# Kernel tuning notes

Measured on AMD Instinct MI355X. Metric: run time of the kernel, lower is better.

The kernel has to match this reference:

```python
import jax, jax.numpy as jnp
import numpy as np

SCALE, K, PATCH, STRIDE = 2, 5, 3, 1
EPS = 1e-5


def im2patch(x, p, s):
    # x: (b,c,H,W) -> (b,c,p,p,m1,m2), 'VALID' patches (padding is 0 for our sizes)
    b, c, H, W = x.shape
    m1 = (H - p) // s + 1
    m2 = (W - p) // s + 1
    ii = (jnp.arange(m1) * s)[:, None] + jnp.arange(p)[None, :]   # (m1,p)
    jj = (jnp.arange(m2) * s)[:, None] + jnp.arange(p)[None, :]   # (m2,p)
    pt = x[:, :, ii[:, :, None, None], jj[None, None, :, :]]      # (b,c,m1,p,m2,p)
    return pt.transpose(0, 1, 3, 5, 2, 4)                         # (b,c,p,p,m1,m2)


def patch2im(patches, p, s):
    # overlap-add fold, averaged by per-pixel patch counts (torch F.fold / ones-fold divisor)
    b, c, _, _, m1, m2 = patches.shape
    Hp = (m1 - 1) * s + p
    Wp = (m2 - 1) * s + p
    out = jnp.zeros((b, c, Hp, Wp), patches.dtype)
    cnt = jnp.zeros((Hp, Wp), patches.dtype)
    for i in range(p):          # fixed small loop over patch offsets (p*p = 36)
        for j in range(p):
            out = out.at[:, :, i:i + s * m1:s, j:j + s * m2:s].add(patches[:, :, i, j])
            cnt = cnt.at[i:i + s * m1:s, j:j + s * m2:s].add(1.0)
    return out / cnt


def setup_inputs():
    key = jax.random.key(0)
    k1, k2, k3 = jax.random.split(key, 3)
    b, cy, H, W = 1, 64, 80, 80
    y = jax.random.normal(k1, (b, cy, H, W), jnp.float32)
    yd = jax.random.normal(k2, (b, cy * SCALE ** 2, H // SCALE, W // SCALE), jnp.float32)
    m = ((H - PATCH) // STRIDE + 1) ** 2
    n = ((H // SCALE - PATCH) // STRIDE + 1) ** 2
    idx_k = jax.random.randint(k3, (b, m, K), 0, n, jnp.int32)
    return {"y": y, "yd": yd, "idx_k": idx_k}


def reference(y, yd, idx_k):
    b, cy, H, W = y.shape
    c = yd.shape[1]           # = cy * scale^2
    rs = SCALE ** 2
    y_p = im2patch(y, PATCH, STRIDE)      # (b,cy,p,p,m1,m2)
    yd_p = im2patch(yd, PATCH, STRIDE)    # (b,c,p,p,n1,n2)
    m1, m2 = y_p.shape[-2:]
    n1, n2 = yd_p.shape[-2:]
    m, n = m1 * m2, n1 * n2
    f = c * PATCH * PATCH
    y_flat = y_p.transpose(0, 4, 5, 1, 2, 3).reshape(b, m, f // rs)
    yd_flat = yd_p.transpose(0, 4, 5, 1, 2, 3).reshape(b, n, f)
    # top-k neighbor gather: (b,n,f)[idx (b,m,k)] -> (b,m,k,f) -> (b,m,f,k)
    z = jax.vmap(lambda t, i: t[i])(yd_flat, idx_k)
    z = z.transpose(0, 1, 3, 2)
    # AdaIN: normalize gathered HR patches, apply LR query patch stats (unbiased var, torch default)
    y_n = y_flat.reshape(b, m, c // rs, PATCH * PATCH)
    z_n = z.reshape(b, m, c // rs, rs * PATCH * PATCH, K)
    z_mu = z_n.mean(axis=3, keepdims=True)
    z_sd = jnp.sqrt(z_n.var(axis=3, ddof=1, keepdims=True) + EPS)
    y_mu = y_n.mean(axis=3, keepdims=True)[..., None]        # (b,m,c',1,1)
    y_sd = jnp.sqrt(y_n.var(axis=3, ddof=1, keepdims=True) + EPS)[..., None]
    z = ((z_n - z_mu) / z_sd * y_sd + y_mu).reshape(b, m, f, K)
    # rearrange f = (cy, scale, scale, p1, p2) into SR patches (b, k*cy, p*scale, p*scale, m1, m2)
    z = z.transpose(0, 3, 2, 1)                                   # (b,k,f,m)
    z = z.reshape(b, K, cy, SCALE, SCALE, PATCH, PATCH, m1, m2)
    z = z.transpose(0, 1, 2, 5, 3, 6, 4, 7, 8)                    # (b,k,cy,p1,s,p2,s,m1,m2)
    z = z.reshape(b, K * cy, PATCH * SCALE, PATCH * SCALE, m1, m2)
    z_sr = patch2im(z, PATCH * SCALE, STRIDE * SCALE)             # (b,k*cy,H*scale,W*scale)
    return z_sr.reshape(b, K * cy, H * SCALE, W * SCALE)
```

## Files before the change

kernel.cpp:

```cpp
#include <hip/hip_runtime.h>
#include <hip/hip_fp16.h>
#include <string.h>

#define CY     64
#define HY     80
#define HD     40
#define SPD    (HD*HD)
#define M1     78
#define N1     38
#define M_TOT  (M1*M1)
#define N_TOT  (N1*N1)
#define KK     5
#define HS     160
#define EPSF   1e-5f
#define LP     17

typedef float f32x2 __attribute__((ext_vector_type(2)));

__device__ __forceinline__ unsigned pkf16(float a, float b) {
    __half2 h = __floats2half2_rn(a, b);
    unsigned u; memcpy(&u, &h, 4); return u;
}
__device__ __forceinline__ f32x2 upk2(unsigned u) {
    __half2 h; memcpy(&h, &u, 4);
    float2 f = __half22float2(h);
    f32x2 r; r.x = f.x; r.y = f.y; return r;
}

__global__ __launch_bounds__(256) void pre_kernel(const float* __restrict__ y,
                                                  const float* __restrict__ yd,
                                                  uint4* __restrict__ ydW,
                                                  unsigned* __restrict__ zstP,
                                                  unsigned* __restrict__ ystP) {
    int id = blockIdx.x * 256 + threadIdx.x;
    if (id < SPD * 64) {
        int cc = id & 63, sp = id >> 6;
        const float* b0 = yd + (cc * 4) * SPD + sp;
        int d = (sp < SPD - 1) ? 1 : 0;
        ydW[sp * 64 + cc] = make_uint4(pkf16(b0[0], b0[SPD]),
                                       pkf16(b0[2*SPD], b0[3*SPD]),
                                       pkf16(b0[d], b0[SPD+d]),
                                       pkf16(b0[2*SPD+d], b0[3*SPD+d]));
        return;
    }
    id -= SPD * 64;
    if (id < N_TOT * 64) {
        int n  = id % N_TOT;
        int cc = id / N_TOT;
        int ni = n / N1, nj = n - ni * N1;
        const float* base = yd + (cc * 4) * SPD + ni * HD + nj;
        float s = 0.f, sq = 0.f;
#pragma unroll
        for (int r = 0; r < 4; ++r)
#pragma unroll
            for (int i = 0; i < 3; ++i)
#pragma unroll
                for (int j = 0; j < 3; ++j) {
                    float v = base[r * SPD + i * HD + j];
                    s += v; sq += v * v;
                }
        float mu  = s * (1.f / 36.f);
        float var = (sq - 36.f * mu * mu) * (1.f / 35.f);
        zstP[n * 64 + cc] = pkf16(mu, rsqrtf(var + EPSF));
        return;
    }
    id -= N_TOT * 64;
    if (id >= CY * M_TOT) return;
    int m  = id % M_TOT;
    int cc = id / M_TOT;
    int mi = m / M1, mj = m - mi * M1;
    const float* base = y + cc * (HY * HY) + mi * HY + mj;
    float s = 0.f, sq = 0.f;
#pragma unroll
    for (int i = 0; i < 3; ++i)
#pragma unroll
        for (int j = 0; j < 3; ++j) {
            float v = base[i * HY + j];
            s += v; sq += v * v;
        }
    float mu  = s * (1.f / 9.f);
    float var = (sq - 9.f * mu * mu) * (1.f / 8.f);
    ystP[m * 64 + cc] = pkf16(mu, sqrtf(var + EPSF));
}

__global__ __launch_bounds__(256) void agg_kernel(
    const uint4* __restrict__ ydW, const unsigned* __restrict__ zstP,
    const unsigned* __restrict__ ystP, const int* __restrict__ idx,
    float* __restrict__ out)
{
    __shared__ float lds[128 * LP];

    int lane = threadIdx.x & 63;
    int w    = __builtin_amdgcn_readfirstlane(threadIdx.x >> 6);
    int bid  = blockIdx.x;
    int wg   = (bid & 7) * 500 + (bid >> 3);
    int k    = wg / 800;
    int rem  = wg - k * 800;
    int y    = rem / 10;
    int xb   = rem - y * 10;
    int x0   = xb * 8 + w * 2;

    f32x2 acc01[2] = {{0.f,0.f},{0.f,0.f}};
    f32x2 acc23[2] = {{0.f,0.f},{0.f,0.f}};
    float bs[2] = {0.f, 0.f};
    float inv0, inv1;

    auto serve = [&](f32x2& a01, f32x2& a23, float& bsum,
                     unsigned lo, unsigned hi, float a, float b) {
        f32x2 am; am.x = a; am.y = a;
        a01 = __builtin_elementwise_fma(am, upk2(lo), a01);
        a23 = __builtin_elementwise_fma(am, upk2(hi), a23);
        bsum += b;
    };

    if (y >= 2 && y <= M1 - 1 && x0 >= 2 && x0 <= M1 - 2) {
        inv0 = inv1 = 1.f / 9.f;
        unsigned ysu[12], zsu[12];
        int nn[12];
#pragma unroll
        for (int p = 0; p < 12; ++p) {
            int m = (y - 2 + (p >> 2)) * M1 + (x0 - 2 + (p & 3));
            nn[p]  = idx[m * KK + k];
            ysu[p] = ystP[m * 64 + lane];
        }
#pragma unroll
        for (int p = 0; p < 12; ++p)
            zsu[p] = zstP[nn[p] * 64 + lane];
        float aa[12], bb[12];
        int spb[12];
#pragma unroll
        for (int p = 0; p < 12; ++p) {
            f32x2 ys = upk2(ysu[p]), zs = upk2(zsu[p]);
            aa[p] = ys.y * zs.y;
            bb[p] = fmaf(-zs.x, aa[p], ys.x);
            int n = nn[p], ni = n / N1;
            spb[p] = ni * HD + (n - ni * N1);
        }
#pragma unroll
        for (int r = 0; r < 3; ++r) {
            int roff = (2 - r) * HD;
            int s0 = spb[r*4+0] + roff, s1 = spb[r*4+1] + roff;
            int s2 = spb[r*4+2] + roff, s3 = spb[r*4+3] + roff;
            uint2 v0 = *(const uint2*)(ydW + (s0 + 2) * 64 + lane);
            uint4 v1 = ydW[(s1 + 1) * 64 + lane];
            uint4 v2 = ydW[(s2 + 0) * 64 + lane];
            uint2 v3 = *(const uint2*)(ydW + (s3 + 0) * 64 + lane);
            serve(acc01[0], acc23[0], bs[0], v0.x, v0.y, aa[r*4+0], bb[r*4+0]);
            serve(acc01[0], acc23[0], bs[0], v1.x, v1.y, aa[r*4+1], bb[r*4+1]);
            serve(acc01[1], acc23[1], bs[1], v1.z, v1.w, aa[r*4+1], bb[r*4+1]);
            serve(acc01[0], acc23[0], bs[0], v2.x, v2.y, aa[r*4+2], bb[r*4+2]);
            serve(acc01[1], acc23[1], bs[1], v2.z, v2.w, aa[r*4+2], bb[r*4+2]);
            serve(acc01[1], acc23[1], bs[1], v3.x, v3.y, aa[r*4+3], bb[r*4+3]);
        }
    } else {
#pragma unroll
        for (int q = 0; q < 2; ++q) {
            int x = x0 + q;
            int milo = max(0, y - 2), mihi = min(M1 - 1, y);
            int mjlo = max(0, x - 2), mjhi = min(M1 - 1, x);
            float iv = 1.f / (float)((mihi - milo + 1) * (mjhi - mjlo + 1));
            if (q == 0) inv0 = iv; else inv1 = iv;
            for (int mi = milo; mi <= mihi; ++mi)
                for (int mj = mjlo; mj <= mjhi; ++mj) {
                    int m = mi * M1 + mj;
                    int n = idx[m * KK + k];
                    f32x2 ys = upk2(ystP[m * 64 + lane]);
                    f32x2 zs = upk2(zstP[n * 64 + lane]);
                    float a = ys.y * zs.y;
                    float b = fmaf(-zs.x, a, ys.x);
                    int ni = n / N1;
                    int sp = ni * HD + (n - ni * N1) + (y - mi) * HD + (x - mj);
                    uint2 v = *(const uint2*)(ydW + sp * 64 + lane);
                    if (q == 0) serve(acc01[0], acc23[0], bs[0], v.x, v.y, a, b);
                    else        serve(acc01[1], acc23[1], bs[1], v.x, v.y, a, b);
                }
        }
    }

#pragma unroll
    for (int q = 0; q < 2; ++q) {
        float iv = q ? inv1 : inv0;
        float bq = bs[q];
        int col = (w * 2 + q) * 2;
        lds[(0 * CY + lane) * LP + col]     = (acc01[q].x + bq) * iv;
        lds[(0 * CY + lane) * LP + col + 1] = (acc01[q].y + bq) * iv;
        lds[(1 * CY + lane) * LP + col]     = (acc23[q].x + bq) * iv;
        lds[(1 * CY + lane) * LP + col + 1] = (acc23[q].y + bq) * iv;
    }

    __syncthreads();

    int q  = lane >> 4;
    int xi = lane & 15;
    int X0 = xb * 16, Y0 = 2 * y;
#pragma unroll
    for (int t = 0; t < 8; ++t) {
        int row = t * 16 + w * 4 + q;
        float v = lds[row * LP + xi];
        int dy = row >> 6, cc = row & 63;
        __builtin_nontemporal_store(v,
            out + (((size_t)(k * CY + cc) * HS + (Y0 + dy)) * HS + X0 + xi));
    }
}

extern "C" void kernel_launch(void* const* d_in, const int* in_sizes, int n_in,
                              void* d_out, int out_size, void* d_ws, size_t ws_size,
                              hipStream_t stream) {
    const float* y   = (const float*)d_in[0];
    const float* yd  = (const float*)d_in[1];
    const int*   idx = (const int*)d_in[2];
    float* out = (float*)d_out;

    char* ws = (char*)d_ws;
    uint4*    ydW  = (uint4*)ws;
    unsigned* zstP = (unsigned*)(ws + 1638400);
    unsigned* ystP = (unsigned*)(ws + 2008064);

    int pre_total = SPD * 64 + N_TOT * 64 + CY * M_TOT;
    pre_kernel<<<(pre_total + 255) / 256, 256, 0, stream>>>(y, yd, ydW, zstP, ystP);
    agg_kernel<<<KK * 800, 256, 0, stream>>>(ydW, zstP, ystP, idx, out);
}
```

Before: 32.40 us.

## Process two row tiles per block with early-issued gathers for the second tile

Each block of the aggregation kernel now handles two output rows (y0 and y0+40), which halves the grid. The index, statistics and feature loads for the second tile are issued before the first tile's compute and store phase, so their latency overlaps with that work. This is meant to hide gather latency and spread block launch overhead over more work. In exchange it raises register pressure, which may lower occupancy, and it adds an extra LDS barrier between the two store phases.

```diff
diff --git a/kernel.cpp b/kernel.cpp
--- a/kernel.cpp
+++ b/kernel.cpp
@@ -93,17 +93,40 @@
     int lane = threadIdx.x & 63;
     int w    = __builtin_amdgcn_readfirstlane(threadIdx.x >> 6);
     int bid  = blockIdx.x;
-    int wg   = (bid & 7) * 500 + (bid >> 3);
-    int k    = wg / 800;
-    int rem  = wg - k * 800;
-    int y    = rem / 10;
-    int xb   = rem - y * 10;
+    int wg   = (bid & 7) * 250 + (bid >> 3);
+    int k    = wg / 400;
+    int rem  = wg - k * 400;
+    int y0   = rem / 10;
+    int xb   = rem - y0 * 10;
     int x0   = xb * 8 + w * 2;
-
-    f32x2 acc01[2] = {{0.f,0.f},{0.f,0.f}};
-    f32x2 acc23[2] = {{0.f,0.f},{0.f,0.f}};
-    float bs[2] = {0.f, 0.f};
-    float inv0, inv1;
+    int yA   = y0, yB = y0 + 40;
+
+    bool fx    = (x0 >= 2 && x0 <= M1 - 2);
+    bool fastA = fx && (yA >= 2) && (yA <= M1 - 1);
+    bool fastB = fx && (yB >= 2) && (yB <= M1 - 1);
+
+    int nnA[12], nnB[12];
+    unsigned ysuA[12], ysuB[12], zsuA[12], zsuB[12];
+    if (fastA) {
+#pragma unroll
+        for (int p = 0; p < 12; ++p) {
+            int m = (yA - 2 + (p >> 2)) * M1 + (x0 - 2 + (p & 3));
+            nnA[p]  = idx[m * KK + k];
+            ysuA[p] = ystP[m * 64 + lane];
+        }
+#pragma unroll
+        for (int p = 0; p < 12; ++p) zsuA[p] = zstP[nnA[p] * 64 + lane];
+    }
+    if (fastB) {
+#pragma unroll
+        for (int p = 0; p < 12; ++p) {
+            int m = (yB - 2 + (p >> 2)) * M1 + (x0 - 2 + (p & 3));
+            nnB[p]  = idx[m * KK + k];
+            ysuB[p] = ystP[m * 64 + lane];
+        }
+#pragma unroll
+        for (int p = 0; p < 12; ++p) zsuB[p] = zstP[nnB[p] * 64 + lane];
+    }
 
     auto serve = [&](f32x2& a01, f32x2& a23, float& bsum,
                      unsigned lo, unsigned hi, float a, float b) {
@@ -113,53 +136,15 @@
         bsum += b;
     };
 
-    if (y >= 2 && y <= M1 - 1 && x0 >= 2 && x0 <= M1 - 2) {
-        inv0 = inv1 = 1.f / 9.f;
-        unsigned ysu[12], zsu[12];
-        int nn[12];
-#pragma unroll
-        for (int p = 0; p < 12; ++p) {
-            int m = (y - 2 + (p >> 2)) * M1 + (x0 - 2 + (p & 3));
-            nn[p]  = idx[m * KK + k];
-            ysu[p] = ystP[m * 64 + lane];
-        }
-#pragma unroll
-        for (int p = 0; p < 12; ++p)
-            zsu[p] = zstP[nn[p] * 64 + lane];
-        float aa[12], bb[12];
-        int spb[12];
-#pragma unroll
-        for (int p = 0; p < 12; ++p) {
-            f32x2 ys = upk2(ysu[p]), zs = upk2(zsu[p]);
-            aa[p] = ys.y * zs.y;
-            bb[p] = fmaf(-zs.x, aa[p], ys.x);
-            int n = nn[p], ni = n / N1;
-            spb[p] = ni * HD + (n - ni * N1);
-        }
-#pragma unroll
-        for (int r = 0; r < 3; ++r) {
-            int roff = (2 - r) * HD;
-            int s0 = spb[r*4+0] + roff, s1 = spb[r*4+1] + roff;
-            int s2 = spb[r*4+2] + roff, s3 = spb[r*4+3] + roff;
-            uint2 v0 = *(const uint2*)(ydW + (s0 + 2) * 64 + lane);
-            uint4 v1 = ydW[(s1 + 1) * 64 + lane];
-            uint4 v2 = ydW[(s2 + 0) * 64 + lane];
-            uint2 v3 = *(const uint2*)(ydW + (s3 + 0) * 64 + lane);
-            serve(acc01[0], acc23[0], bs[0], v0.x, v0.y, aa[r*4+0], bb[r*4+0]);
-            serve(acc01[0], acc23[0], bs[0], v1.x, v1.y, aa[r*4+1], bb[r*4+1]);
-            serve(acc01[1], acc23[1], bs[1], v1.z, v1.w, aa[r*4+1], bb[r*4+1]);
-            serve(acc01[0], acc23[0], bs[0], v2.x, v2.y, aa[r*4+2], bb[r*4+2]);
-            serve(acc01[1], acc23[1], bs[1], v2.z, v2.w, aa[r*4+2], bb[r*4+2]);
-            serve(acc01[1], acc23[1], bs[1], v3.x, v3.y, aa[r*4+3], bb[r*4+3]);
-        }
-    } else {
+    auto slow_tile = [&](int yt, f32x2 a01[2], f32x2 a23[2], float bs[2],
+                         float& i0, float& i1) {
 #pragma unroll
         for (int q = 0; q < 2; ++q) {
             int x = x0 + q;
-            int milo = max(0, y - 2), mihi = min(M1 - 1, y);
+            int milo = max(0, yt - 2), mihi = min(M1 - 1, yt);
             int mjlo = max(0, x - 2), mjhi = min(M1 - 1, x);
             float iv = 1.f / (float)((mihi - milo + 1) * (mjhi - mjlo + 1));
-            if (q == 0) inv0 = iv; else inv1 = iv;
+            if (q == 0) i0 = iv; else i1 = iv;
             for (int mi = milo; mi <= mihi; ++mi)
                 for (int mj = mjlo; mj <= mjhi; ++mj) {
                     int m = mi * M1 + mj;
@@ -169,37 +154,148 @@
                     float a = ys.y * zs.y;
                     float b = fmaf(-zs.x, a, ys.x);
                     int ni = n / N1;
-                    int sp = ni * HD + (n - ni * N1) + (y - mi) * HD + (x - mj);
+                    int sp = ni * HD + (n - ni * N1) + (yt - mi) * HD + (x - mj);
                     uint2 v = *(const uint2*)(ydW + sp * 64 + lane);
-                    if (q == 0) serve(acc01[0], acc23[0], bs[0], v.x, v.y, a, b);
-                    else        serve(acc01[1], acc23[1], bs[1], v.x, v.y, a, b);
+                    if (q == 0) serve(a01[0], a23[0], bs[0], v.x, v.y, a, b);
+                    else        serve(a01[1], a23[1], bs[1], v.x, v.y, a, b);
                 }
         }
-    }
-
-#pragma unroll
-    for (int q = 0; q < 2; ++q) {
-        float iv = q ? inv1 : inv0;
-        float bq = bs[q];
-        int col = (w * 2 + q) * 2;
-        lds[(0 * CY + lane) * LP + col]     = (acc01[q].x + bq) * iv;
-        lds[(0 * CY + lane) * LP + col + 1] = (acc01[q].y + bq) * iv;
-        lds[(1 * CY + lane) * LP + col]     = (acc23[q].x + bq) * iv;
-        lds[(1 * CY + lane) * LP + col + 1] = (acc23[q].y + bq) * iv;
-    }
-
-    __syncthreads();
-
-    int q  = lane >> 4;
-    int xi = lane & 15;
-    int X0 = xb * 16, Y0 = 2 * y;
-#pragma unroll
-    for (int t = 0; t < 8; ++t) {
-        int row = t * 16 + w * 4 + q;
-        float v = lds[row * LP + xi];
-        int dy = row >> 6, cc = row & 63;
-        __builtin_nontemporal_store(v,
-            out + (((size_t)(k * CY + cc) * HS + (Y0 + dy)) * HS + X0 + xi));
+    };
+
+    f32x2 accA01[2] = {{0.f,0.f},{0.f,0.f}};
+    f32x2 accA23[2] = {{0.f,0.f},{0.f,0.f}};
+    float bsA[2] = {0.f, 0.f};
+    float invA0 = 1.f / 9.f, invA1 = 1.f / 9.f;
+    if (fastA) {
+        int spbA[12];
+#pragma unroll
+        for (int p = 0; p < 12; ++p) {
+            int n = nnA[p], ni = n / N1;
+            spbA[p] = ni * HD + (n - ni * N1);
+        }
+        uint2 Aw0[3], Aw3[3]; uint4 Au1[3], Au2[3];
+#pragma unroll
+        for (int r = 0; r < 3; ++r) {
+            int roff = (2 - r) * HD;
+            Aw0[r] = *(const uint2*)(ydW + (spbA[r*4+0] + roff + 2) * 64 + lane);
+            Au1[r] = ydW[(spbA[r*4+1] + roff + 1) * 64 + lane];
+            Au2[r] = ydW[(spbA[r*4+2] + roff + 0) * 64 + lane];
+            Aw3[r] = *(const uint2*)(ydW + (spbA[r*4+3] + roff + 0) * 64 + lane);
+        }
+#pragma unroll
+        for (int r = 0; r < 3; ++r) {
+            float aa0, bb0, aa1, bb1, aa2, bb2, aa3, bb3;
+            { f32x2 ys = upk2(ysuA[r*4+0]), zs = upk2(zsuA[r*4+0]);
+              aa0 = ys.y * zs.y; bb0 = fmaf(-zs.x, aa0, ys.x); }
+            { f32x2 ys = upk2(ysuA[r*4+1]), zs = upk2(zsuA[r*4+1]);
+              aa1 = ys.y * zs.y; bb1 = fmaf(-zs.x, aa1, ys.x); }
+            { f32x2 ys = upk2(ysuA[r*4+2]), zs = upk2(zsuA[r*4+2]);
+              aa2 = ys.y * zs.y; bb2 = fmaf(-zs.x, aa2, ys.x); }
+            { f32x2 ys = upk2(ysuA[r*4+3]), zs = upk2(zsuA[r*4+3]);
+              aa3 = ys.y * zs.y; bb3 = fmaf(-zs.x, aa3, ys.x); }
+            serve(accA01[0], accA23[0], bsA[0], Aw0[r].x, Aw0[r].y, aa0, bb0);
+            serve(accA01[0], accA23[0], bsA[0], Au1[r].x, Au1[r].y, aa1, bb1);
+            serve(accA01[1], accA23[1], bsA[1], Au1[r].z, Au1[r].w, aa1, bb1);
+            serve(accA01[0], accA23[0], bsA[0], Au2[r].x, Au2[r].y, aa2, bb2);
+            serve(accA01[1], accA23[1], bsA[1], Au2[r].z, Au2[r].w, aa2, bb2);
+            serve(accA01[1], accA23[1], bsA[1], Aw3[r].x, Aw3[r].y, aa3, bb3);
+        }
+    } else {
+        slow_tile(yA, accA01, accA23, bsA, invA0, invA1);
+    }
+
+    uint2 Bw0[3], Bw3[3]; uint4 Bu1[3], Bu2[3];
+    if (fastB) {
+        int spbB[12];
+#pragma unroll
+        for (int p = 0; p < 12; ++p) {
+            int n = nnB[p], ni = n / N1;
+            spbB[p] = ni * HD + (n - ni * N1);
+        }
+#pragma unroll
+        for (int r = 0; r < 3; ++r) {
+            int roff = (2 - r) * HD;
+            Bw0[r] = *(const uint2*)(ydW + (spbB[r*4+0] + roff + 2) * 64 + lane);
+            Bu1[r] = ydW[(spbB[r*4+1] + roff + 1) * 64 + lane];
+            Bu2[r] = ydW[(spbB[r*4+2] + roff + 0) * 64 + lane];
+            Bw3[r] = *(const uint2*)(ydW + (spbB[r*4+3] + roff + 0) * 64 + lane);
+        }
+    }
+
+    {
+#pragma unroll
+        for (int q = 0; q < 2; ++q) {
+            float iv = q ? invA1 : invA0;
+            float bq = bsA[q];
+            int col = (w * 2 + q) * 2;
+            lds[(0 * CY + lane) * LP + col]     = (accA01[q].x + bq) * iv;
+            lds[(0 * CY + lane) * LP + col + 1] = (accA01[q].y + bq) * iv;
+            lds[(1 * CY + lane) * LP + col]     = (accA23[q].x + bq) * iv;
+            lds[(1 * CY + lane) * LP + col + 1] = (accA23[q].y + bq) * iv;
+        }
+        __syncthreads();
+        int q = lane >> 4, xi = lane & 15;
+        int X0 = xb * 16, Y0 = 2 * yA;
+#pragma unroll
+        for (int t = 0; t < 8; ++t) {
+            int row = t * 16 + w * 4 + q;
+            float v = lds[row * LP + xi];
+            int dy = row >> 6, cc = row & 63;
+            __builtin_nontemporal_store(v,
+                out + (((size_t)(k * CY + cc) * HS + (Y0 + dy)) * HS + X0 + xi));
+        }
+        __syncthreads();
+    }
+
+    f32x2 accB01[2] = {{0.f,0.f},{0.f,0.f}};
+    f32x2 accB23[2] = {{0.f,0.f},{0.f,0.f}};
+    float bsB[2] = {0.f, 0.f};
+    float invB0 = 1.f / 9.f, invB1 = 1.f / 9.f;
+    if (fastB) {
+#pragma unroll
+        for (int r = 0; r < 3; ++r) {
+            float aa0, bb0, aa1, bb1, aa2, bb2, aa3, bb3;
+            { f32x2 ys = upk2(ysuB[r*4+0]), zs = upk2(zsuB[r*4+0]);
+              aa0 = ys.y * zs.y; bb0 = fmaf(-zs.x, aa0, ys.x); }
+            { f32x2 ys = upk2(ysuB[r*4+1]), zs = upk2(zsuB[r*4+1]);
+              aa1 = ys.y * zs.y; bb1 = fmaf(-zs.x, aa1, ys.x); }
+            { f32x2 ys = upk2(ysuB[r*4+2]), zs = upk2(zsuB[r*4+2]);
+              aa2 = ys.y * zs.y; bb2 = fmaf(-zs.x, aa2, ys.x); }
+            { f32x2 ys = upk2(ysuB[r*4+3]), zs = upk2(zsuB[r*4+3]);
+              aa3 = ys.y * zs.y; bb3 = fmaf(-zs.x, aa3, ys.x); }
+            serve(accB01[0], accB23[0], bsB[0], Bw0[r].x, Bw0[r].y, aa0, bb0);
+            serve(accB01[0], accB23[0], bsB[0], Bu1[r].x, Bu1[r].y, aa1, bb1);
+            serve(accB01[1], accB23[1], bsB[1], Bu1[r].z, Bu1[r].w, aa1, bb1);
+            serve(accB01[0], accB23[0], bsB[0], Bu2[r].x, Bu2[r].y, aa2, bb2);
+            serve(accB01[1], accB23[1], bsB[1], Bu2[r].z, Bu2[r].w, aa2, bb2);
+            serve(accB01[1], accB23[1], bsB[1], Bw3[r].x, Bw3[r].y, aa3, bb3);
+        }
+    } else {
+        slow_tile(yB, accB01, accB23, bsB, invB0, invB1);
+    }
+
+    {
+#pragma unroll
+        for (int q = 0; q < 2; ++q) {
+            float iv = q ? invB1 : invB0;
+            float bq = bsB[q];
+            int col = (w * 2 + q) * 2;
+            lds[(0 * CY + lane) * LP + col]     = (accB01[q].x + bq) * iv;
+            lds[(0 * CY + lane) * LP + col + 1] = (accB01[q].y + bq) * iv;
+            lds[(1 * CY + lane) * LP + col]     = (accB23[q].x + bq) * iv;
+            lds[(1 * CY + lane) * LP + col + 1] = (accB23[q].y + bq) * iv;
+        }
+        __syncthreads();
+        int q = lane >> 4, xi = lane & 15;
+        int X0 = xb * 16, Y0 = 2 * yB;
+#pragma unroll
+        for (int t = 0; t < 8; ++t) {
+            int row = t * 16 + w * 4 + q;
+            float v = lds[row * LP + xi];
+            int dy = row >> 6, cc = row & 63;
+            __builtin_nontemporal_store(v,
+                out + (((size_t)(k * CY + cc) * HS + (Y0 + dy)) * HS + X0 + xi));
+        }
     }
 }
 
@@ -218,5 +314,5 @@
 
     int pre_total = SPD * 64 + N_TOT * 64 + CY * M_TOT;
     pre_kernel<<<(pre_total + 255) / 256, 256, 0, stream>>>(y, yd, ydW, zstP, ystP);
-    agg_kernel<<<KK * 800, 256, 0, stream>>>(ydW, zstP, ystP, idx, out);
-}
+    agg_kernel<<<KK * 400, 256, 0, stream>>>(ydW, zstP, ystP, idx, out);
+}
```

New measurement: 35.64 us. 1.1x slower.

## Process two neighbor ranks per workgroup to share query stats and reduce blocks

Applied to the files above, without the earlier changes.

Each workgroup of the aggregation kernel now handles two of the K neighbor indices (the last group handles one), so the ystP query-statistics loads and the index arithmetic are shared across both. The grid shrinks from 4000 to 2400 blocks and the LDS tile doubles to hold both outputs. The cost is higher register pressure from doubled accumulators and in-flight gathers, which may lower occupancy, and an uneven load between the two-rank and one-rank blocks.

```diff
diff --git a/kernel.cpp b/kernel.cpp
--- a/kernel.cpp
+++ b/kernel.cpp
@@ -83,123 +83,161 @@
     ystP[m * 64 + cc] = pkf16(mu, sqrtf(var + EPSF));
 }
 
+template<int NK>
+__device__ __forceinline__ void tile_run(
+    int lane, int w, int k0, int y, int x0,
+    const uint4* __restrict__ ydW, const unsigned* __restrict__ zstP,
+    const unsigned* __restrict__ ystP, const int* __restrict__ idx,
+    float* lds, float inv[2])
+{
+    f32x2 acc01[NK][2], acc23[NK][2];
+    float bs[NK][2];
+#pragma unroll
+    for (int kk = 0; kk < NK; ++kk)
+#pragma unroll
+        for (int q = 0; q < 2; ++q) {
+            acc01[kk][q].x = 0.f; acc01[kk][q].y = 0.f;
+            acc23[kk][q].x = 0.f; acc23[kk][q].y = 0.f;
+            bs[kk][q] = 0.f;
+        }
+
+    auto serve = [&](int kk, int q, unsigned lo, unsigned hi, float a, float b) {
+        f32x2 am; am.x = a; am.y = a;
+        acc01[kk][q] = __builtin_elementwise_fma(am, upk2(lo), acc01[kk][q]);
+        acc23[kk][q] = __builtin_elementwise_fma(am, upk2(hi), acc23[kk][q]);
+        bs[kk][q] += b;
+    };
+
+    if (y >= 2 && y <= M1 - 1 && x0 >= 2 && x0 <= M1 - 2) {
+        inv[0] = inv[1] = 1.f / 9.f;
+        int nn[NK][12];
+        unsigned ysu[12];
+#pragma unroll
+        for (int p = 0; p < 12; ++p) {
+            int m = (y - 2 + (p >> 2)) * M1 + (x0 - 2 + (p & 3));
+#pragma unroll
+            for (int kk = 0; kk < NK; ++kk) nn[kk][p] = idx[m * KK + k0 + kk];
+            ysu[p] = ystP[m * 64 + lane];
+        }
+#pragma unroll
+        for (int r = 0; r < 3; ++r) {
+            int roff = (2 - r) * HD;
+            unsigned zsu[NK][4];
+            uint2 v0[NK], v3[NK]; uint4 u1[NK], u2[NK];
+#pragma unroll
+            for (int kk = 0; kk < NK; ++kk) {
+                int n0 = nn[kk][r*4+0], n1 = nn[kk][r*4+1];
+                int n2 = nn[kk][r*4+2], n3 = nn[kk][r*4+3];
+                int s0 = (n0 / N1) * HD + (n0 - (n0 / N1) * N1) + roff;
+                int s1 = (n1 / N1) * HD + (n1 - (n1 / N1) * N1) + roff;
+                int s2 = (n2 / N1) * HD + (n2 - (n2 / N1) * N1) + roff;
+                int s3 = (n3 / N1) * HD + (n3 - (n3 / N1) * N1) + roff;
+                v0[kk] = *(const uint2*)(ydW + (s0 + 2) * 64 + lane);
+                u1[kk] = ydW[(s1 + 1) * 64 + lane];
+                u2[kk] = ydW[(s2 + 0) * 64 + lane];
+                v3[kk] = *(const uint2*)(ydW + (s3 + 0) * 64 + lane);
+                zsu[kk][0] = zstP[n0 * 64 + lane];
+                zsu[kk][1] = zstP[n1 * 64 + lane];
+                zsu[kk][2] = zstP[n2 * 64 + lane];
+                zsu[kk][3] = zstP[n3 * 64 + lane];
+            }
+#pragma unroll
+            for (int kk = 0; kk < NK; ++kk) {
+                float aa[4], bb[4];
+#pragma unroll
+                for (int c = 0; c < 4; ++c) {
+                    f32x2 ys = upk2(ysu[r*4+c]), zs = upk2(zsu[kk][c]);
+                    aa[c] = ys.y * zs.y;
+                    bb[c] = fmaf(-zs.x, aa[c], ys.x);
+                }
+                serve(kk, 0, v0[kk].x, v0[kk].y, aa[0], bb[0]);
+                serve(kk, 0, u1[kk].x, u1[kk].y, aa[1], bb[1]);
+                serve(kk, 1, u1[kk].z, u1[kk].w, aa[1], bb[1]);
+                serve(kk, 0, u2[kk].x, u2[kk].y, aa[2], bb[2]);
+                serve(kk, 1, u2[kk].z, u2[kk].w, aa[2], bb[2]);
+                serve(kk, 1, v3[kk].x, v3[kk].y, aa[3], bb[3]);
+            }
+        }
+    } else {
+#pragma unroll
+        for (int q = 0; q < 2; ++q) {
+            int x = x0 + q;
+            int milo = max(0, y - 2), mihi = min(M1 - 1, y);
+            int mjlo = max(0, x - 2), mjhi = min(M1 - 1, x);
+            inv[q] = 1.f / (float)((mihi - milo + 1) * (mjhi - mjlo + 1));
+            for (int mi = milo; mi <= mihi; ++mi)
+                for (int mj = mjlo; mj <= mjhi; ++mj) {
+                    int m = mi * M1 + mj;
+                    unsigned ysuv = ystP[m * 64 + lane];
+#pragma unroll
+                    for (int kk = 0; kk < NK; ++kk) {
+                        int n = idx[m * KK + k0 + kk];
+                        f32x2 ys = upk2(ysuv);
+                        f32x2 zs = upk2(zstP[n * 64 + lane]);
+                        float a = ys.y * zs.y;
+                        float b = fmaf(-zs.x, a, ys.x);
+                        int ni = n / N1;
+                        int sp = ni * HD + (n - ni * N1) + (y - mi) * HD + (x - mj);
+                        uint2 v = *(const uint2*)(ydW + sp * 64 + lane);
+                        serve(kk, q, v.x, v.y, a, b);
+                    }
+                }
+        }
+    }
+
+#pragma unroll
+    for (int kk = 0; kk < NK; ++kk)
+#pragma unroll
+        for (int q = 0; q < 2; ++q) {
+            float iv = inv[q];
+            float bq = bs[kk][q];
+            int col = (w * 2 + q) * 2;
+            lds[((kk * 2 + 0) * CY + lane) * LP + col]     = (acc01[kk][q].x + bq) * iv;
+            lds[((kk * 2 + 0) * CY + lane) * LP + col + 1] = (acc01[kk][q].y + bq) * iv;
+            lds[((kk * 2 + 1) * CY + lane) * LP + col]     = (acc23[kk][q].x + bq) * iv;
+            lds[((kk * 2 + 1) * CY + lane) * LP + col + 1] = (acc23[kk][q].y + bq) * iv;
+        }
+}
+
 __global__ __launch_bounds__(256) void agg_kernel(
     const uint4* __restrict__ ydW, const unsigned* __restrict__ zstP,
     const unsigned* __restrict__ ystP, const int* __restrict__ idx,
     float* __restrict__ out)
 {
-    __shared__ float lds[128 * LP];
+    __shared__ float lds[256 * LP];
 
     int lane = threadIdx.x & 63;
     int w    = __builtin_amdgcn_readfirstlane(threadIdx.x >> 6);
     int bid  = blockIdx.x;
-    int wg   = (bid & 7) * 500 + (bid >> 3);
-    int k    = wg / 800;
-    int rem  = wg - k * 800;
+    int wg   = (bid & 7) * 300 + (bid >> 3);
+    int kp   = wg / 800;
+    int rem  = wg - kp * 800;
     int y    = rem / 10;
     int xb   = rem - y * 10;
     int x0   = xb * 8 + w * 2;
-
-    f32x2 acc01[2] = {{0.f,0.f},{0.f,0.f}};
-    f32x2 acc23[2] = {{0.f,0.f},{0.f,0.f}};
-    float bs[2] = {0.f, 0.f};
-    float inv0, inv1;
-
-    auto serve = [&](f32x2& a01, f32x2& a23, float& bsum,
-                     unsigned lo, unsigned hi, float a, float b) {
-        f32x2 am; am.x = a; am.y = a;
-        a01 = __builtin_elementwise_fma(am, upk2(lo), a01);
-        a23 = __builtin_elementwise_fma(am, upk2(hi), a23);
-        bsum += b;
-    };
-
-    if (y >= 2 && y <= M1 - 1 && x0 >= 2 && x0 <= M1 - 2) {
-        inv0 = inv1 = 1.f / 9.f;
-        unsigned ysu[12], zsu[12];
-        int nn[12];
-#pragma unroll
-        for (int p = 0; p < 12; ++p) {
-            int m = (y - 2 + (p >> 2)) * M1 + (x0 - 2 + (p & 3));
-            nn[p]  = idx[m * KK + k];
-            ysu[p] = ystP[m * 64 + lane];
-        }
-#pragma unroll
-        for (int p = 0; p < 12; ++p)
-            zsu[p] = zstP[nn[p] * 64 + lane];
-        float aa[12], bb[12];
-        int spb[12];
-#pragma unroll
-        for (int p = 0; p < 12; ++p) {
-            f32x2 ys = upk2(ysu[p]), zs = upk2(zsu[p]);
-            aa[p] = ys.y * zs.y;
-            bb[p] = fmaf(-zs.x, aa[p], ys.x);
-            int n = nn[p], ni = n / N1;
-            spb[p] = ni * HD + (n - ni * N1);
-        }
-#pragma unroll
-        for (int r = 0; r < 3; ++r) {
-            int roff = (2 - r) * HD;
-            int s0 = spb[r*4+0] + roff, s1 = spb[r*4+1] + roff;
-            int s2 = spb[r*4+2] + roff, s3 = spb[r*4+3] + roff;
-            uint2 v0 = *(const uint2*)(ydW + (s0 + 2) * 64 + lane);
-            uint4 v1 = ydW[(s1 + 1) * 64 + lane];
-            uint4 v2 = ydW[(s2 + 0) * 64 + lane];
-            uint2 v3 = *(const uint2*)(ydW + (s3 + 0) * 64 + lane);
-            serve(acc01[0], acc23[0], bs[0], v0.x, v0.y, aa[r*4+0], bb[r*4+0]);
-            serve(acc01[0], acc23[0], bs[0], v1.x, v1.y, aa[r*4+1], bb[r*4+1]);
-            serve(acc01[1], acc23[1], bs[1], v1.z, v1.w, aa[r*4+1], bb[r*4+1]);
-            serve(acc01[0], acc23[0], bs[0], v2.x, v2.y, aa[r*4+2], bb[r*4+2]);
-            serve(acc01[1], acc23[1], bs[1], v2.z, v2.w, aa[r*4+2], bb[r*4+2]);
-            serve(acc01[1], acc23[1], bs[1], v3.x, v3.y, aa[r*4+3], bb[r*4+3]);
-        }
+    int k0   = kp * 2;
+
+    float inv[2];
+    int nk;
+    if (kp < 2) {
+        tile_run<2>(lane, w, k0, y, x0, ydW, zstP, ystP, idx, lds, inv);
+        nk = 2;
     } else {
-#pragma unroll
-        for (int q = 0; q < 2; ++q) {
-            int x = x0 + q;
-            int milo = max(0, y - 2), mihi = min(M1 - 1, y);
-            int mjlo = max(0, x - 2), mjhi = min(M1 - 1, x);
-            float iv = 1.f / (float)((mihi - milo + 1) * (mjhi - mjlo + 1));
-            if (q == 0) inv0 = iv; else inv1 = iv;
-            for (int mi = milo; mi <= mihi; ++mi)
-                for (int mj = mjlo; mj <= mjhi; ++mj) {
-                    int m = mi * M1 + mj;
-                    int n = idx[m * KK + k];
-                    f32x2 ys = upk2(ystP[m * 64 + lane]);
-                    f32x2 zs = upk2(zstP[n * 64 + lane]);
-                    float a = ys.y * zs.y;
-                    float b = fmaf(-zs.x, a, ys.x);
-                    int ni = n / N1;
-                    int sp = ni * HD + (n - ni * N1) + (y - mi) * HD + (x - mj);
-                    uint2 v = *(const uint2*)(ydW + sp * 64 + lane);
-                    if (q == 0) serve(acc01[0], acc23[0], bs[0], v.x, v.y, a, b);
-                    else        serve(acc01[1], acc23[1], bs[1], v.x, v.y, a, b);
-                }
-        }
-    }
-
-#pragma unroll
-    for (int q = 0; q < 2; ++q) {
-        float iv = q ? inv1 : inv0;
-        float bq = bs[q];
-        int col = (w * 2 + q) * 2;
-        lds[(0 * CY + lane) * LP + col]     = (acc01[q].x + bq) * iv;
-        lds[(0 * CY + lane) * LP + col + 1] = (acc01[q].y + bq) * iv;
-        lds[(1 * CY + lane) * LP + col]     = (acc23[q].x + bq) * iv;
-        lds[(1 * CY + lane) * LP + col + 1] = (acc23[q].y + bq) * iv;
+        tile_run<1>(lane, w, k0, y, x0, ydW, zstP, ystP, idx, lds, inv);
+        nk = 1;
     }
 
     __syncthreads();
 
-    int q  = lane >> 4;
+    int qg = lane >> 4;
     int xi = lane & 15;
     int X0 = xb * 16, Y0 = 2 * y;
-#pragma unroll
-    for (int t = 0; t < 8; ++t) {
-        int row = t * 16 + w * 4 + q;
+    for (int t = 0; t < nk * 8; ++t) {
+        int row = t * 16 + w * 4 + qg;
         float v = lds[row * LP + xi];
-        int dy = row >> 6, cc = row & 63;
+        int kk = row >> 7, dy = (row >> 6) & 1, cc = row & 63;
         __builtin_nontemporal_store(v,
-            out + (((size_t)(k * CY + cc) * HS + (Y0 + dy)) * HS + X0 + xi));
+            out + (((size_t)((k0 + kk) * CY + cc) * HS + (Y0 + dy)) * HS + X0 + xi));
     }
 }
 
@@ -218,5 +256,5 @@
 
     int pre_total = SPD * 64 + N_TOT * 64 + CY * M_TOT;
     pre_kernel<<<(pre_total + 255) / 256, 256, 0, stream>>>(y, yd, ydW, zstP, ystP);
-    agg_kernel<<<KK * 800, 256, 0, stream>>>(ydW, zstP, ystP, idx, out);
-}
+    agg_kernel<<<3 * 800, 256, 0, stream>>>(ydW, zstP, ystP, idx, out);
+}
```

Measured after the change: 34.11 us. 1.05x slower.
